# Kernel optimization log

Hardware: AMD Instinct MI355X
Metric: run time of the kernel (lower is better)

The kernel has to match this reference:

```python
import jax, jax.numpy as jnp
import numpy as np

NUM_USERS = 100000
NUM_POIS = 50000
N = NUM_USERS + NUM_POIS   # total graph nodes (users then pois)
D = 128                    # embedding_dim
POI_D = 320                # poi_embed_dim
E = 2000000                # number of edges
B = 1024                   # batch of user ids
NEG_SLOPE = 0.2


def setup_inputs() -> dict:
    key = jax.random.key(0)
    ks = jax.random.split(key, 12)
    stdv = 1.0 / np.sqrt(D)  # module resets all params to U(-stdv, stdv)
    u = lambda k, s: jax.random.uniform(k, s, jnp.float32, -stdv, stdv)
    return {
        "user_idx": jax.random.randint(ks[0], (B,), 0, NUM_USERS),
        "poi_embeddings": jax.random.normal(ks[1], (NUM_POIS, POI_D), jnp.float32),
        "edge_index": jax.random.randint(ks[2], (2, E), 0, N),
        "user_table": u(ks[3], (NUM_USERS, D)),
        "Wp": u(ks[4], (POI_D, D)), "bp": u(ks[5], (D,)),
        "W1": u(ks[6], (D, D)), "b1": u(ks[7], (D,)),
        "W2": u(ks[8], (D, D)), "b2": u(ks[9], (D,)),
        "Wf": u(ks[10], (D, D)), "bf": u(ks[11], (D,)),
    }


def _leaky(x):
    return jnp.where(x >= 0, x, NEG_SLOPE * x)


def _gcn_conv(x, W, b, src, dst, dinv):
    # PyG GCNConv: h = xW; out_i = sum_{j->i} dinv_j*dinv_i*h_j + dinv_i^2*h_i + b
    h = x @ W
    norm = dinv[src] * dinv[dst]                       # [E]
    agg = jax.ops.segment_sum(h[src] * norm[:, None], dst, num_segments=N)
    agg = agg + (dinv * dinv)[:, None] * h             # self-loop term
    return agg + b


def reference(user_idx, poi_embeddings, edge_index, user_table,
              Wp, bp, W1, b1, W2, b2, Wf, bf):
    src, dst = edge_index[0], edge_index[1]
    # degree with self-loops (edge weight 1)
    deg = 1.0 + jax.ops.segment_sum(jnp.ones((E,), jnp.float32), dst, num_segments=N)
    dinv = jax.lax.rsqrt(deg)

    poi_feats = poi_embeddings @ Wp + bp               # [NUM_POIS, D]
    x = jnp.concatenate([user_table, poi_feats], axis=0)  # [N, D]
    x = _leaky(_gcn_conv(x, W1, b1, src, dst, dinv))
    # dropout p=0.2 is identity in eval mode
    x = _leaky(_gcn_conv(x, W2, b2, src, dst, dinv))

    out = x[user_idx] + user_table[user_idx]           # [B, D]
    return out @ Wf + bf
```

## Files before the change

kernel.cpp:

```cpp
#include <hip/hip_runtime.h>

#define NUSERS 100000
#define NPOIS  50000
#define NN     150000
#define DD     128
#define EE     2000000
#define BB     1024
#define NT2M   32768

#define CH_IPT 16
#define CH_BLK 256
#define CHUNK  (CH_IPT * CH_BLK)

#define HR   3
#define HS   50000
#define HSI  12500
#define HC   85
#define HPER 23532

typedef __attribute__((ext_vector_type(8))) short short8;
typedef __attribute__((ext_vector_type(4))) float f32x4;
typedef unsigned short ushort_t;

__device__ __forceinline__ ushort_t f2bf(float x) {
    union { float f; unsigned u; } a; a.f = x;
    unsigned r = a.u + 0x7fffu + ((a.u >> 16) & 1u);
    return (ushort_t)(r >> 16);
}
__device__ __forceinline__ float bf2f(ushort_t h) {
    union { unsigned u; float f; } a; a.u = ((unsigned)h) << 16;
    return a.f;
}

__global__ void k_mark(const int* __restrict__ uidx, int* __restrict__ mask_s2,
                       int* __restrict__ mask_t2) {
    int b = blockIdx.x * blockDim.x + threadIdx.x;
    if (b < BB) { int u = uidx[b]; mask_s2[u] = 1; mask_t2[u] = 1; }
}

__global__ void k_markT2(const int* __restrict__ src, const int* __restrict__ dst,
                         const int* __restrict__ mask_s2, int* __restrict__ mask_t2) {
    const int nq = EE / 4;
    int stride = gridDim.x * blockDim.x;
    for (int q = blockIdx.x * blockDim.x + threadIdx.x; q < nq; q += stride) {
        int4 d4 = *(const int4*)&dst[q << 2];
        int m0 = mask_s2[d4.x], m1 = mask_s2[d4.y];
        int m2 = mask_s2[d4.z], m3 = mask_s2[d4.w];
        if (m0 | m1 | m2 | m3) {
            int4 s4 = *(const int4*)&src[q << 2];
            if (m0) mask_t2[s4.x] = 1;
            if (m1) mask_t2[s4.y] = 1;
            if (m2) mask_t2[s4.z] = 1;
            if (m3) mask_t2[s4.w] = 1;
        }
    }
}

__global__ __launch_bounds__(1024)
void k_hist3(const int* __restrict__ dst, int* __restrict__ slab) {
    __shared__ int h[HSI];
    const int r = blockIdx.x / HC, c = blockIdx.x % HC;
    const int lo = r * HS;
    const int tid = threadIdx.x;
    for (int i = tid; i < HSI; i += 1024) h[i] = 0;
    __syncthreads();
    const int e0 = c * HPER;
    const int e1 = min(e0 + HPER, EE);
    for (int e = e0 + tid * 4; e < e1; e += 4096) {
        int4 d4 = *(const int4*)&dst[e];
        unsigned u0 = (unsigned)(d4.x - lo), u1 = (unsigned)(d4.y - lo);
        unsigned u2 = (unsigned)(d4.z - lo), u3 = (unsigned)(d4.w - lo);
        if (u0 < (unsigned)HS) atomicAdd(&h[u0 >> 2], 1 << ((u0 & 3) << 3));
        if (u1 < (unsigned)HS) atomicAdd(&h[u1 >> 2], 1 << ((u1 & 3) << 3));
        if (u2 < (unsigned)HS) atomicAdd(&h[u2 >> 2], 1 << ((u2 & 3) << 3));
        if (u3 < (unsigned)HS) atomicAdd(&h[u3 >> 2], 1 << ((u3 & 3) << 3));
    }
    __syncthreads();
    int* out = slab + (size_t)blockIdx.x * HSI;
    for (int i = tid; i < HSI; i += 1024) out[i] = h[i];
}

__global__ void k_reduce3(const int* __restrict__ slab, int* __restrict__ cnt,
                          float* __restrict__ dinv) {
    int i = blockIdx.x * blockDim.x + threadIdx.x;
    if (i >= HR * HSI) return;
    int r = i / HSI, ii = i - r * HSI;
    const int* p = slab + (size_t)(r * HC) * HSI + ii;
    int s = 0;
    #pragma unroll
    for (int c = 0; c < HC; ++c) s += p[(size_t)c * HSI];
    int n0 = r * HS + (ii << 2);
    int4 cv;
    cv.x = s & 255; cv.y = (s >> 8) & 255; cv.z = (s >> 16) & 255; cv.w = (s >> 24) & 255;
    *(int4*)&cnt[n0] = cv;
    float4 dv;
    dv.x = rsqrtf(1.0f + (float)cv.x); dv.y = rsqrtf(1.0f + (float)cv.y);
    dv.z = rsqrtf(1.0f + (float)cv.z); dv.w = rsqrtf(1.0f + (float)cv.w);
    *(float4*)&dinv[n0] = dv;
}

__global__ __launch_bounds__(256)
void k_slots(const int* __restrict__ mask_s2, const int* __restrict__ mask_t2,
             int* __restrict__ slot_s2, int* __restrict__ slot_t2,
             int* __restrict__ rev_s2, int* __restrict__ rev_t2,
             int* __restrict__ ctr) {
    __shared__ int s_wcnt_t[4], s_wcnt_s[4];
    __shared__ int s_base_t, s_base_s;
    const int tid = threadIdx.x;
    const int lane = tid & 63;
    const int wid = tid >> 6;
    const int nch = (NN + CHUNK - 1) / CHUNK;
    for (int c = blockIdx.x; c < nch; c += gridDim.x) {
        const int n0 = c * CHUNK;
        unsigned hbits_t = 0, hbits_s = 0;
        int wt = 0, ws = 0;
        #pragma unroll
        for (int i = 0; i < CH_IPT; ++i) {
            int n = n0 + i * CH_BLK + tid;
            bool inb = (n < NN);
            bool ht = inb && (mask_t2[n] != 0);
            bool hs = inb && (mask_s2[n] != 0);
            unsigned long long mt = __ballot(ht);
            unsigned long long ms = __ballot(hs);
            if (ht) hbits_t |= (1u << i);
            if (hs) hbits_s |= (1u << i);
            wt += __popcll(mt); ws += __popcll(ms);
        }
        if (lane == 0) { s_wcnt_t[wid] = wt; s_wcnt_s[wid] = ws; }
        __syncthreads();
        if (tid == 0) s_base_t = atomicAdd(&ctr[0], s_wcnt_t[0]+s_wcnt_t[1]+s_wcnt_t[2]+s_wcnt_t[3]);
        if (tid == 1) s_base_s = atomicAdd(&ctr[1], s_wcnt_s[0]+s_wcnt_s[1]+s_wcnt_s[2]+s_wcnt_s[3]);
        __syncthreads();
        int off_t = s_base_t, off_s = s_base_s;
        for (int w = 0; w < wid; ++w) { off_t += s_wcnt_t[w]; off_s += s_wcnt_s[w]; }
        #pragma unroll
        for (int i = 0; i < CH_IPT; ++i) {
            unsigned long long mt = __ballot((hbits_t >> i) & 1);
            unsigned long long ms = __ballot((hbits_s >> i) & 1);
            int n = n0 + i * CH_BLK + tid;
            if ((hbits_t >> i) & 1) {
                int p = off_t + __popcll(mt & ((1ull << lane) - 1ull));
                slot_t2[n] = p; rev_t2[p] = n;
            }
            if ((hbits_s >> i) & 1) {
                int p = off_s + __popcll(ms & ((1ull << lane) - 1ull));
                slot_s2[n] = p; rev_s2[p] = n;
            }
            off_t += __popcll(mt); off_s += __popcll(ms);
        }
        __syncthreads();
    }
}

__global__ __launch_bounds__(1024)
void k_scan2(const int* __restrict__ ctr, const int* __restrict__ rev_t2,
             const int* __restrict__ rev_s2, const int* __restrict__ cnt,
             int* __restrict__ ptr1, int* __restrict__ cur1, int* __restrict__ cur1b,
             int* __restrict__ ptr2, int* __restrict__ cur2, int* __restrict__ cur2b) {
    __shared__ int wsum[16];
    __shared__ int s_carry;
    const int which = blockIdx.x;
    const int n = ctr[which];
    const int* rev = which ? rev_s2 : rev_t2;
    int* ptr = which ? ptr2 : ptr1;
    int* cur = which ? cur2 : cur1;
    int* curB = which ? cur2b : cur1b;
    const int tid = threadIdx.x;
    const int lane = tid & 63, wid = tid >> 6;
    if (tid == 0) s_carry = 0;
    __syncthreads();
    for (int base = 0; base < n; base += 4096) {
        int i0 = base + tid * 4;
        int v[4];
        #pragma unroll
        for (int k = 0; k < 4; ++k) {
            int i = i0 + k;
            v[k] = (i < n) ? cnt[rev[i]] : 0;
        }
        int tsum = v[0] + v[1] + v[2] + v[3];
        int x = tsum;
        #pragma unroll
        for (int s = 1; s < 64; s <<= 1) {
            int y = __shfl_up(x, s, 64);
            if (lane >= s) x += y;
        }
        if (lane == 63) wsum[wid] = x;
        __syncthreads();
        if (wid == 0) {
            int wv = (lane < 16) ? wsum[lane] : 0;
            #pragma unroll
            for (int s = 1; s < 16; s <<= 1) {
                int y = __shfl_up(wv, s, 64);
                if (lane >= s) wv += y;
            }
            if (lane < 16) wsum[lane] = wv;
        }
        __syncthreads();
        int carry = s_carry;
        int woff = (wid > 0) ? wsum[wid - 1] : 0;
        int excl = carry + woff + (x - tsum);
        #pragma unroll
        for (int k = 0; k < 4; ++k) {
            int i = i0 + k;
            if (i < n) { ptr[i] = excl; cur[i] = excl; curB[i] = excl + v[k]; }
            excl += v[k];
        }
        __syncthreads();
        if (tid == 0) s_carry = carry + wsum[15];
        __syncthreads();
    }
}

__global__ void k_scatter(const int* __restrict__ src, const int* __restrict__ dst,
                          const int* __restrict__ mask_s2, const int* __restrict__ mask_t2,
                          const int* __restrict__ slot_s2, const int* __restrict__ slot_t2,
                          int* __restrict__ cur1, int* __restrict__ cur1b,
                          int* __restrict__ cur2,
                          int* __restrict__ csr1, int* __restrict__ csr2) {
    int stride = gridDim.x * blockDim.x;
    for (int e = blockIdx.x * blockDim.x + threadIdx.x; e < EE; e += stride) {
        int d = dst[e];
        bool t = (mask_t2[d] != 0);
        bool s2 = (mask_s2[d] != 0);
        if (t | s2) {
            int s = src[e];
            if (t) {
                int sl = slot_t2[d];
                if (s < NUSERS) { int p = atomicAdd(&cur1[sl], 1);  csr1[p] = s; }
                else            { int p = atomicAdd(&cur1b[sl], -1); csr1[p - 1] = s; }
            }
            if (s2) { int p = atomicAdd(&cur2[slot_s2[d]], 1); csr2[p] = s; }
        }
    }
}

__global__ void k_wpw1(const float* __restrict__ Wp, const float* __restrict__ W1,
                       float* __restrict__ WpW1) {
    int i = blockIdx.x * blockDim.x + threadIdx.x;
    if (i >= 320 * 128) return;
    int r = i >> 7, c = i & 127;
    float s = 0.f;
    for (int k = 0; k < 128; ++k) s = fmaf(Wp[r * 128 + k], W1[k * 128 + c], s);
    WpW1[i] = s;
}

__global__ void k_bpw1(const float* __restrict__ bp, const float* __restrict__ W1,
                       float* __restrict__ bpW1) {
    int c = threadIdx.x;
    float s = 0.f;
    for (int k = 0; k < 128; ++k) s = fmaf(bp[k], W1[k * 128 + c], s);
    bpW1[c] = s;
}

__global__ void k_wprepW(const float* __restrict__ W1, const float* __restrict__ WpW1,
                         const float* __restrict__ bpW1,
                         ushort_t* __restrict__ Th, ushort_t* __restrict__ Tl) {
    int i = blockIdx.x * blockDim.x + threadIdx.x;
    if (i >= 128 * 512) return;
    int n = i >> 9, k = i & 511;
    float x = (k < 128) ? W1[k * 128 + n]
            : (k < 448) ? WpW1[(k - 128) * 128 + n]
            : (k == 448) ? bpW1[n] : 0.f;
    ushort_t h = f2bf(x);
    ushort_t l = f2bf(x - bf2f(h));
    Th[n * 512 + k] = h; Tl[n * 512 + k] = l;
}

__global__ void k_wprep2(const float* __restrict__ W2, const float* __restrict__ Wf,
                         ushort_t* __restrict__ T2h, ushort_t* __restrict__ T2l,
                         ushort_t* __restrict__ Tfh, ushort_t* __restrict__ Tfl) {
    int i = blockIdx.x * blockDim.x + threadIdx.x;
    if (i >= 2 * 128 * 128) return;
    int wsel = i >> 14, j = i & 16383;
    const float* W = wsel ? Wf : W2;
    ushort_t* Th = wsel ? Tfh : T2h;
    ushort_t* Tl = wsel ? Tfl : T2l;
    int k = j >> 7, n = j & 127;
    float x = W[j];
    ushort_t h = f2bf(x);
    ushort_t l = f2bf(x - bf2f(h));
    Th[n * 128 + k] = h; Tl[n * 128 + k] = l;
}

__global__ __launch_bounds__(256)
void k_agg1(const int* __restrict__ ctr, const int* __restrict__ rev_t2,
            const int* __restrict__ ptr1, const int* __restrict__ cur1,
            const int* __restrict__ cnt, const int* __restrict__ csr1,
            const float* __restrict__ dinv,
            const float* __restrict__ ut, const float* __restrict__ poi,
            ushort_t* __restrict__ Ah, ushort_t* __restrict__ Al) {
    const int nt2 = min(ctr[0], NT2M);
    const int lane = threadIdx.x & 63;
    const int w0 = (blockIdx.x * blockDim.x + threadIdx.x) >> 6;
    const int nw = (gridDim.x * blockDim.x) >> 6;
    for (int slot = w0; slot < nt2; slot += nw) {
        int node = rev_t2[slot];
        float dn = dinv[node], dd = dn * dn;
        float u0 = 0.f, u1 = 0.f, p0 = 0.f, p1 = 0.f, p2 = 0.f, p3 = 0.f, p4 = 0.f, sP = 0.f;
        if (node < NUSERS) {
            const float2 v = *(const float2*)&ut[((size_t)node << 7) + (lane << 1)];
            u0 = dd * v.x; u1 = dd * v.y;
        } else {
            const float* pr = poi + (size_t)(node - NUSERS) * 320;
            p0 = dd * pr[lane]; p1 = dd * pr[lane + 64]; p2 = dd * pr[lane + 128];
            p3 = dd * pr[lane + 192]; p4 = dd * pr[lane + 256];
            sP = dd;
        }
        const int j0 = ptr1[slot];
        const int sp = cur1[slot];
        const int jend = j0 + cnt[node];
        int j = j0;
        for (; j + 4 <= sp; j += 4) {
            int s0 = csr1[j], s1 = csr1[j + 1], s2 = csr1[j + 2], s3 = csr1[j + 3];
            float w0 = dinv[s0] * dn, w1 = dinv[s1] * dn;
            float w2 = dinv[s2] * dn, w3 = dinv[s3] * dn;
            const float2 v0 = *(const float2*)&ut[((size_t)s0 << 7) + (lane << 1)];
            const float2 v1 = *(const float2*)&ut[((size_t)s1 << 7) + (lane << 1)];
            const float2 v2 = *(const float2*)&ut[((size_t)s2 << 7) + (lane << 1)];
            const float2 v3 = *(const float2*)&ut[((size_t)s3 << 7) + (lane << 1)];
            u0 = fmaf(w0, v0.x, u0); u1 = fmaf(w0, v0.y, u1);
            u0 = fmaf(w1, v1.x, u0); u1 = fmaf(w1, v1.y, u1);
            u0 = fmaf(w2, v2.x, u0); u1 = fmaf(w2, v2.y, u1);
            u0 = fmaf(w3, v3.x, u0); u1 = fmaf(w3, v3.y, u1);
        }
        for (; j < sp; ++j) {
            int s = csr1[j];
            float w = dinv[s] * dn;
            const float2 v = *(const float2*)&ut[((size_t)s << 7) + (lane << 1)];
            u0 = fmaf(w, v.x, u0); u1 = fmaf(w, v.y, u1);
        }
        for (j = sp; j + 2 <= jend; j += 2) {
            int s0 = csr1[j], s1 = csr1[j + 1];
            float w0 = dinv[s0] * dn, w1 = dinv[s1] * dn;
            const float* pa = poi + (size_t)(s0 - NUSERS) * 320;
            const float* pb = poi + (size_t)(s1 - NUSERS) * 320;
            p0 = fmaf(w0, pa[lane], p0);       p1 = fmaf(w0, pa[lane + 64], p1);
            p2 = fmaf(w0, pa[lane + 128], p2); p3 = fmaf(w0, pa[lane + 192], p3);
            p4 = fmaf(w0, pa[lane + 256], p4);
            p0 = fmaf(w1, pb[lane], p0);       p1 = fmaf(w1, pb[lane + 64], p1);
            p2 = fmaf(w1, pb[lane + 128], p2); p3 = fmaf(w1, pb[lane + 192], p3);
            p4 = fmaf(w1, pb[lane + 256], p4);
            sP += w0 + w1;
        }
        for (; j < jend; ++j) {
            int s = csr1[j];
            float w = dinv[s] * dn;
            const float* pr = poi + (size_t)(s - NUSERS) * 320;
            p0 = fmaf(w, pr[lane], p0);       p1 = fmaf(w, pr[lane + 64], p1);
            p2 = fmaf(w, pr[lane + 128], p2); p3 = fmaf(w, pr[lane + 192], p3);
            p4 = fmaf(w, pr[lane + 256], p4);
            sP += w;
        }
        size_t base = (size_t)slot << 9;
        ushort_t h, l;
        h = f2bf(u0); l = f2bf(u0 - bf2f(h));
        Ah[base + (lane << 1)] = h; Al[base + (lane << 1)] = l;
        h = f2bf(u1); l = f2bf(u1 - bf2f(h));
        Ah[base + (lane << 1) + 1] = h; Al[base + (lane << 1) + 1] = l;
        float pv[5] = {p0, p1, p2, p3, p4};
        #pragma unroll
        for (int q = 0; q < 5; ++q) {
            h = f2bf(pv[q]); l = f2bf(pv[q] - bf2f(h));
            Ah[base + 128 + lane + (q << 6)] = h; Al[base + 128 + lane + (q << 6)] = l;
        }
        float t = (lane == 0) ? sP : 0.f;
        h = f2bf(t); l = f2bf(t - bf2f(h));
        Ah[base + 448 + lane] = h; Al[base + 448 + lane] = l;
    }
}

template<int KSTEPS, bool LEAKY>
__global__ __launch_bounds__(256)
void gemm_bf(const ushort_t* __restrict__ Ah_g, const ushort_t* __restrict__ Al_g,
             const ushort_t* __restrict__ BTh, const ushort_t* __restrict__ BTl,
             const float* __restrict__ bias, float* __restrict__ C,
             int M, const int* __restrict__ Mdyn)
{
    constexpr int K = KSTEPS * 64;
    __shared__ ushort_t Bh[128 * 64], Bl[128 * 64];
    __shared__ ushort_t Ahs[64 * 64], Als[64 * 64];
    const int tid = threadIdx.x;
    const int wave = tid >> 6, lane = tid & 63;
    const int wr = wave >> 1, wc = wave & 1;
    const int lr = lane & 15, g = lane >> 4;
    if (Mdyn) M = min(*Mdyn, NT2M);
    const int ntiles = (M + 63) >> 6;
    for (int tile = blockIdx.x; tile < ntiles; tile += gridDim.x) {
        const int row0 = tile << 6;
        f32x4 acc[2][4];
        #pragma unroll
        for (int a = 0; a < 2; ++a)
            #pragma unroll
            for (int b = 0; b < 4; ++b) acc[a][b] = (f32x4){0.f, 0.f, 0.f, 0.f};
        for (int kc = 0; kc < K; kc += 64) {
            __syncthreads();
            #pragma unroll
            for (int i = 0; i < 4; ++i) {
                int c = tid + i * 256;
                int n = c >> 3, kq = c & 7;
                size_t go = (size_t)n * K + kc + kq * 8;
                int boff = n * 128 + ((kq * 16) ^ ((n & 7) << 4));
                *(int4*)((char*)Bh + boff) = *(const int4*)&BTh[go];
                *(int4*)((char*)Bl + boff) = *(const int4*)&BTl[go];
            }
            #pragma unroll
            for (int i = 0; i < 2; ++i) {
                int c = tid + i * 256;
                int r = c >> 3, kq = c & 7;
                int row = row0 + r;
                int4 va = {0, 0, 0, 0}, vb = {0, 0, 0, 0};
                if (row < M) {
                    size_t go = (size_t)row * K + kc + kq * 8;
                    va = *(const int4*)&Ah_g[go];
                    vb = *(const int4*)&Al_g[go];
                }
                int aoff = r * 128 + ((kq * 16) ^ ((r & 7) << 4));
                *(int4*)((char*)Ahs + aoff) = va;
                *(int4*)((char*)Als + aoff) = vb;
            }
            __syncthreads();
            #pragma unroll
            for (int kk2 = 0; kk2 < 2; ++kk2) {
                short8 afh[2], afl[2];
                #pragma unroll
                for (int rt = 0; rt < 2; ++rt) {
                    int ar = wr * 32 + rt * 16 + lr;
                    int off = ar * 128 + ((kk2 * 64 + g * 16) ^ ((ar & 7) << 4));
                    afh[rt] = *(short8*)((char*)Ahs + off);
                    afl[rt] = *(short8*)((char*)Als + off);
                }
                #pragma unroll
                for (int ct = 0; ct < 4; ++ct) {
                    int bn = wc * 64 + ct * 16 + lr;
                    int off = bn * 128 + ((kk2 * 64 + g * 16) ^ ((bn & 7) << 4));
                    short8 bfh = *(short8*)((char*)Bh + off);
                    short8 bfl = *(short8*)((char*)Bl + off);
                    #pragma unroll
                    for (int rt = 0; rt < 2; ++rt) {
                        acc[rt][ct] = __builtin_amdgcn_mfma_f32_16x16x32_bf16(afh[rt], bfh, acc[rt][ct], 0, 0, 0);
                        acc[rt][ct] = __builtin_amdgcn_mfma_f32_16x16x32_bf16(afh[rt], bfl, acc[rt][ct], 0, 0, 0);
                        acc[rt][ct] = __builtin_amdgcn_mfma_f32_16x16x32_bf16(afl[rt], bfh, acc[rt][ct], 0, 0, 0);
                    }
                }
            }
        }
        #pragma unroll
        for (int ct = 0; ct < 4; ++ct) {
            int col = wc * 64 + ct * 16 + lr;
            float bv = bias[col];
            #pragma unroll
            for (int rt = 0; rt < 2; ++rt) {
                #pragma unroll
                for (int v = 0; v < 4; ++v) {
                    int row = row0 + wr * 32 + rt * 16 + g * 4 + v;
                    if (row < M) {
                        float o = acc[rt][ct][v] + bv;
                        if (LEAKY) o = o >= 0.f ? o : 0.2f * o;
                        C[(size_t)row * 128 + col] = o;
                    }
                }
            }
        }
    }
}

__global__ __launch_bounds__(256)
void k_agg2(const int* __restrict__ ctr, const int* __restrict__ rev_s2,
            const int* __restrict__ ptr2, const int* __restrict__ cnt,
            const int* __restrict__ csr2, const int* __restrict__ slot_t2,
            const float* __restrict__ dinv, const float* __restrict__ x1c,
            ushort_t* __restrict__ X2h, ushort_t* __restrict__ X2l) {
    const int ns2 = ctr[1];
    const int lane = threadIdx.x & 63;
    const int col = lane << 1;
    const int w0 = (blockIdx.x * blockDim.x + threadIdx.x) >> 6;
    const int nw = (gridDim.x * blockDim.x) >> 6;
    for (int slot = w0; slot < ns2; slot += nw) {
        int node = rev_s2[slot];
        float dn = dinv[node], dd = dn * dn;
        float2 acc = *(const float2*)&x1c[((size_t)slot_t2[node] << 7) + col];
        acc.x *= dd; acc.y *= dd;
        const int j0 = ptr2[slot];
        const int jend = j0 + cnt[node];
        int j = j0;
        for (; j + 4 <= jend; j += 4) {
            int s0 = csr2[j], s1 = csr2[j + 1], s2 = csr2[j + 2], s3 = csr2[j + 3];
            float w0 = dinv[s0] * dn, w1 = dinv[s1] * dn;
            float w2 = dinv[s2] * dn, w3 = dinv[s3] * dn;
            const float2 h0 = *(const float2*)&x1c[((size_t)slot_t2[s0] << 7) + col];
            const float2 h1 = *(const float2*)&x1c[((size_t)slot_t2[s1] << 7) + col];
            const float2 h2 = *(const float2*)&x1c[((size_t)slot_t2[s2] << 7) + col];
            const float2 h3 = *(const float2*)&x1c[((size_t)slot_t2[s3] << 7) + col];
            acc.x = fmaf(w0, h0.x, acc.x); acc.y = fmaf(w0, h0.y, acc.y);
            acc.x = fmaf(w1, h1.x, acc.x); acc.y = fmaf(w1, h1.y, acc.y);
            acc.x = fmaf(w2, h2.x, acc.x); acc.y = fmaf(w2, h2.y, acc.y);
            acc.x = fmaf(w3, h3.x, acc.x); acc.y = fmaf(w3, h3.y, acc.y);
        }
        for (; j < jend; ++j) {
            int s = csr2[j];
            float w = dinv[s] * dn;
            const float2 h = *(const float2*)&x1c[((size_t)slot_t2[s] << 7) + col];
            acc.x = fmaf(w, h.x, acc.x);
            acc.y = fmaf(w, h.y, acc.y);
        }
        size_t base = ((size_t)slot << 7) + col;
        ushort_t h0 = f2bf(acc.x), l0 = f2bf(acc.x - bf2f(h0));
        ushort_t h1 = f2bf(acc.y), l1 = f2bf(acc.y - bf2f(h1));
        X2h[base] = h0; X2h[base + 1] = h1;
        X2l[base] = l0; X2l[base + 1] = l1;
    }
}

__global__ void k_finalA(const int* __restrict__ uidx, const int* __restrict__ slot_s2,
                         const float* __restrict__ x2c, const float* __restrict__ ut,
                         ushort_t* __restrict__ Fh, ushort_t* __restrict__ Fl) {
    int i = blockIdx.x * blockDim.x + threadIdx.x;
    if (i >= BB * 64) return;
    int b = i >> 6, l = i & 63;
    int u = uidx[b];
    const float2 xv = *(const float2*)&x2c[((size_t)slot_s2[u] << 7) + (l << 1)];
    const float2 uv = *(const float2*)&ut[((size_t)u << 7) + (l << 1)];
    float a0 = xv.x + uv.x, a1 = xv.y + uv.y;
    size_t base = ((size_t)b << 7) + (l << 1);
    ushort_t h0 = f2bf(a0), l0 = f2bf(a0 - bf2f(h0));
    ushort_t h1 = f2bf(a1), l1 = f2bf(a1 - bf2f(h1));
    Fh[base] = h0; Fh[base + 1] = h1;
    Fl[base] = l0; Fl[base + 1] = l1;
}

extern "C" void kernel_launch(void* const* d_in, const int* in_sizes, int n_in,
                              void* d_out, int out_size, void* d_ws, size_t ws_size,
                              hipStream_t stream) {
    const int*   uidx    = (const int*)d_in[0];
    const float* poi     = (const float*)d_in[1];
    const int*   src     = (const int*)d_in[2];
    const int*   dst     = ((const int*)d_in[2]) + EE;
    const float* usert   = (const float*)d_in[3];
    const float* Wp      = (const float*)d_in[4];
    const float* bp      = (const float*)d_in[5];
    const float* W1      = (const float*)d_in[6];
    const float* b1      = (const float*)d_in[7];
    const float* W2      = (const float*)d_in[8];
    const float* b2      = (const float*)d_in[9];
    const float* Wf      = (const float*)d_in[10];
    const float* bf      = (const float*)d_in[11];
    float* out = (float*)d_out;

    char* w = (char*)d_ws;
    size_t off = 0;
    auto alloc = [&](size_t bytes) -> void* {
        void* p = w + off;
        off = (off + bytes + 255) & ~(size_t)255;
        return p;
    };
    float* dinv    = (float*)alloc((size_t)NN * 4);
    int*   cnt     = (int*)  alloc((size_t)NN * 4);
    int*   mask_s2 = (int*)  alloc((size_t)NN * 4);
    int*   mask_t2 = (int*)  alloc((size_t)NN * 4);
    int*   slot_s2 = (int*)  alloc((size_t)NN * 4);
    int*   slot_t2 = (int*)  alloc((size_t)NN * 4);
    int*   rev_t2  = (int*)  alloc((size_t)NN * 4);
    int*   rev_s2  = (int*)  alloc((size_t)BB * 4);
    int*   ptr1    = (int*)  alloc((size_t)(NN + 1) * 4);
    int*   cur1    = (int*)  alloc((size_t)(NN + 1) * 4);
    int*   cur1b   = (int*)  alloc((size_t)(NN + 1) * 4);
    int*   ptr2    = (int*)  alloc((size_t)(BB + 2) * 4);
    int*   cur2    = (int*)  alloc((size_t)(BB + 2) * 4);
    int*   cur2b   = (int*)  alloc((size_t)(BB + 2) * 4);
    int*   ctr     = (int*)  alloc(256);
    int*   csr1    = (int*)  alloc((size_t)EE * 4);
    int*   csr2    = (int*)  alloc((size_t)EE * 4);
    int*   slab    = (int*)  alloc((size_t)HR * HC * HSI * 4);
    float* WpW1    = (float*)alloc((size_t)320 * 128 * 4);
    float* bpW1    = (float*)alloc((size_t)128 * 4);
    ushort_t* WTh  = (ushort_t*)alloc((size_t)128 * 512 * 2);
    ushort_t* WTl  = (ushort_t*)alloc((size_t)128 * 512 * 2);
    ushort_t* W2Th = (ushort_t*)alloc((size_t)128 * 128 * 2);
    ushort_t* W2Tl = (ushort_t*)alloc((size_t)128 * 128 * 2);
    ushort_t* WfTh = (ushort_t*)alloc((size_t)128 * 128 * 2);
    ushort_t* WfTl = (ushort_t*)alloc((size_t)128 * 128 * 2);
    ushort_t* Ah   = (ushort_t*)alloc((size_t)NT2M * 512 * 2);
    ushort_t* Al   = (ushort_t*)alloc((size_t)NT2M * 512 * 2);
    float* x1c     = (float*)alloc((size_t)NT2M * 128 * 4);
    ushort_t* X2h  = (ushort_t*)alloc((size_t)2048 * 128 * 2);
    ushort_t* X2l  = (ushort_t*)alloc((size_t)2048 * 128 * 2);
    float* x2c     = (float*)alloc((size_t)2048 * 128 * 4);
    ushort_t* Fh   = (ushort_t*)alloc((size_t)BB * 128 * 2);
    ushort_t* Fl   = (ushort_t*)alloc((size_t)BB * 128 * 2);
    if (off > ws_size) return;

    hipMemsetAsync(mask_s2, 0, (size_t)NN * 4, stream);
    hipMemsetAsync(mask_t2, 0, (size_t)NN * 4, stream);
    hipMemsetAsync(ctr, 0, 256, stream);

    k_wpw1  <<<160, 256, 0, stream>>>(Wp, W1, WpW1);
    k_bpw1  <<<1, 128, 0, stream>>>(bp, W1, bpW1);
    k_wprepW<<<256, 256, 0, stream>>>(W1, WpW1, bpW1, WTh, WTl);
    k_wprep2<<<128, 256, 0, stream>>>(W2, Wf, W2Th, W2Tl, WfTh, WfTl);

    k_mark   <<<(BB + 255) / 256, 256, 0, stream>>>(uidx, mask_s2, mask_t2);
    k_markT2 <<<2048, 256, 0, stream>>>(src, dst, mask_s2, mask_t2);
    k_hist3  <<<HR * HC, 1024, 0, stream>>>(dst, slab);
    k_reduce3<<<(HR * HSI + 255) / 256, 256, 0, stream>>>(slab, cnt, dinv);

    k_slots<<<(NN + CHUNK - 1) / CHUNK, 256, 0, stream>>>(mask_s2, mask_t2, slot_s2, slot_t2,
                                                          rev_s2, rev_t2, ctr);
    k_scan2<<<2, 1024, 0, stream>>>(ctr, rev_t2, rev_s2, cnt,
                                    ptr1, cur1, cur1b, ptr2, cur2, cur2b);
    k_scatter<<<2048, 256, 0, stream>>>(src, dst, mask_s2, mask_t2, slot_s2, slot_t2,
                                        cur1, cur1b, cur2, csr1, csr2);

    k_agg1<<<2048, 256, 0, stream>>>(ctr, rev_t2, ptr1, cur1, cnt, csr1, dinv,
                                     usert, poi, Ah, Al);
    gemm_bf<8, true><<<240, 256, 0, stream>>>(Ah, Al, WTh, WTl, b1, x1c, 0, ctr + 0);

    k_agg2<<<256, 256, 0, stream>>>(ctr, rev_s2, ptr2, cnt, csr2, slot_t2, dinv, x1c, X2h, X2l);
    gemm_bf<2, true><<<16, 256, 0, stream>>>(X2h, X2l, W2Th, W2Tl, b2, x2c, 0, ctr + 1);

    k_finalA<<<(BB * 64 + 255) / 256, 256, 0, stream>>>(uidx, slot_s2, x2c, usert, Fh, Fl);
    gemm_bf<2, false><<<16, 256, 0, stream>>>(Fh, Fl, WfTh, WfTl, bf, out, BB, nullptr);
}
```

Measured before the change: 195.7 us.

## Fuse T2 marking into histogram kernel and use slot sentinels in scatter

Removes the standalone k_markT2 pass and folds the mask_s2->mask_t2 propagation into k_hist3. Each of its three row-blocks handles a third of its edge chunk, which saves one launch and reuses the dst stream the kernel already reads. k_scatter now reads slot_t2/slot_s2 directly, with slots memset to -1 beforehand, so the mask lookups go away. This relies on k_slots writing slots only for marked nodes. The aggregation loops drop their scalar tail loops in favour of clamped, predicated 4-wide (or 3-wide for POIs) bodies. Risks include two extra 600KB memsets and some wasted loads on padded lanes.

```diff
diff --git a/kernel.cpp b/kernel.cpp
--- a/kernel.cpp
+++ b/kernel.cpp
@@ -38,26 +38,10 @@
     if (b < BB) { int u = uidx[b]; mask_s2[u] = 1; mask_t2[u] = 1; }
 }
 
-__global__ void k_markT2(const int* __restrict__ src, const int* __restrict__ dst,
-                         const int* __restrict__ mask_s2, int* __restrict__ mask_t2) {
-    const int nq = EE / 4;
-    int stride = gridDim.x * blockDim.x;
-    for (int q = blockIdx.x * blockDim.x + threadIdx.x; q < nq; q += stride) {
-        int4 d4 = *(const int4*)&dst[q << 2];
-        int m0 = mask_s2[d4.x], m1 = mask_s2[d4.y];
-        int m2 = mask_s2[d4.z], m3 = mask_s2[d4.w];
-        if (m0 | m1 | m2 | m3) {
-            int4 s4 = *(const int4*)&src[q << 2];
-            if (m0) mask_t2[s4.x] = 1;
-            if (m1) mask_t2[s4.y] = 1;
-            if (m2) mask_t2[s4.z] = 1;
-            if (m3) mask_t2[s4.w] = 1;
-        }
-    }
-}
-
 __global__ __launch_bounds__(1024)
-void k_hist3(const int* __restrict__ dst, int* __restrict__ slab) {
+void k_hist3(const int* __restrict__ src, const int* __restrict__ dst,
+             const int* __restrict__ mask_s2, int* __restrict__ mask_t2,
+             int* __restrict__ slab) {
     __shared__ int h[HSI];
     const int r = blockIdx.x / HC, c = blockIdx.x % HC;
     const int lo = r * HS;
@@ -74,6 +58,20 @@
         if (u1 < (unsigned)HS) atomicAdd(&h[u1 >> 2], 1 << ((u1 & 3) << 3));
         if (u2 < (unsigned)HS) atomicAdd(&h[u2 >> 2], 1 << ((u2 & 3) << 3));
         if (u3 < (unsigned)HS) atomicAdd(&h[u3 >> 2], 1 << ((u3 & 3) << 3));
+    }
+    const int m0 = e0 + r * (HPER / 3);
+    const int m1 = min(e0 + (r + 1) * (HPER / 3), EE);
+    for (int e = m0 + tid * 4; e < m1; e += 4096) {
+        int4 d4 = *(const int4*)&dst[e];
+        int q0 = mask_s2[d4.x], q1 = mask_s2[d4.y];
+        int q2 = mask_s2[d4.z], q3 = mask_s2[d4.w];
+        if (q0 | q1 | q2 | q3) {
+            int4 s4 = *(const int4*)&src[e];
+            if (q0) mask_t2[s4.x] = 1;
+            if (q1) mask_t2[s4.y] = 1;
+            if (q2) mask_t2[s4.z] = 1;
+            if (q3) mask_t2[s4.w] = 1;
+        }
     }
     __syncthreads();
     int* out = slab + (size_t)blockIdx.x * HSI;
@@ -212,7 +210,6 @@
 }
 
 __global__ void k_scatter(const int* __restrict__ src, const int* __restrict__ dst,
-                          const int* __restrict__ mask_s2, const int* __restrict__ mask_t2,
                           const int* __restrict__ slot_s2, const int* __restrict__ slot_t2,
                           int* __restrict__ cur1, int* __restrict__ cur1b,
                           int* __restrict__ cur2,
@@ -220,16 +217,17 @@
     int stride = gridDim.x * blockDim.x;
     for (int e = blockIdx.x * blockDim.x + threadIdx.x; e < EE; e += stride) {
         int d = dst[e];
-        bool t = (mask_t2[d] != 0);
-        bool s2 = (mask_s2[d] != 0);
-        if (t | s2) {
-            int s = src[e];
-            if (t) {
-                int sl = slot_t2[d];
-                if (s < NUSERS) { int p = atomicAdd(&cur1[sl], 1);  csr1[p] = s; }
-                else            { int p = atomicAdd(&cur1b[sl], -1); csr1[p - 1] = s; }
-            }
-            if (s2) { int p = atomicAdd(&cur2[slot_s2[d]], 1); csr2[p] = s; }
+        int sl1 = slot_t2[d];
+        int sl2 = slot_s2[d];
+        if ((sl1 | sl2) != -1 || sl1 >= 0 || sl2 >= 0) {
+            if (sl1 >= 0 || sl2 >= 0) {
+                int s = src[e];
+                if (sl1 >= 0) {
+                    if (s < NUSERS) { int p = atomicAdd(&cur1[sl1], 1);   csr1[p] = s; }
+                    else            { int p = atomicAdd(&cur1b[sl1], -1); csr1[p - 1] = s; }
+                }
+                if (sl2 >= 0) { int p = atomicAdd(&cur2[sl2], 1); csr2[p] = s; }
+            }
         }
     }
 }
@@ -291,9 +289,9 @@
             ushort_t* __restrict__ Ah, ushort_t* __restrict__ Al) {
     const int nt2 = min(ctr[0], NT2M);
     const int lane = threadIdx.x & 63;
-    const int w0 = (blockIdx.x * blockDim.x + threadIdx.x) >> 6;
+    const int w0id = (blockIdx.x * blockDim.x + threadIdx.x) >> 6;
     const int nw = (gridDim.x * blockDim.x) >> 6;
-    for (int slot = w0; slot < nt2; slot += nw) {
+    for (int slot = w0id; slot < nt2; slot += nw) {
         int node = rev_t2[slot];
         float dn = dinv[node], dd = dn * dn;
         float u0 = 0.f, u1 = 0.f, p0 = 0.f, p1 = 0.f, p2 = 0.f, p3 = 0.f, p4 = 0.f, sP = 0.f;
@@ -309,11 +307,13 @@
         const int j0 = ptr1[slot];
         const int sp = cur1[slot];
         const int jend = j0 + cnt[node];
-        int j = j0;
-        for (; j + 4 <= sp; j += 4) {
-            int s0 = csr1[j], s1 = csr1[j + 1], s2 = csr1[j + 2], s3 = csr1[j + 3];
-            float w0 = dinv[s0] * dn, w1 = dinv[s1] * dn;
-            float w2 = dinv[s2] * dn, w3 = dinv[s3] * dn;
+        for (int j = j0; j < sp; j += 4) {
+            int i1 = min(j + 1, sp - 1), i2 = min(j + 2, sp - 1), i3 = min(j + 3, sp - 1);
+            int s0 = csr1[j], s1 = csr1[i1], s2 = csr1[i2], s3 = csr1[i3];
+            float w0 = dn * dinv[s0];
+            float w1 = (j + 1 < sp) ? dn * dinv[s1] : 0.f;
+            float w2 = (j + 2 < sp) ? dn * dinv[s2] : 0.f;
+            float w3 = (j + 3 < sp) ? dn * dinv[s3] : 0.f;
             const float2 v0 = *(const float2*)&ut[((size_t)s0 << 7) + (lane << 1)];
             const float2 v1 = *(const float2*)&ut[((size_t)s1 << 7) + (lane << 1)];
             const float2 v2 = *(const float2*)&ut[((size_t)s2 << 7) + (lane << 1)];
@@ -323,33 +323,25 @@
             u0 = fmaf(w2, v2.x, u0); u1 = fmaf(w2, v2.y, u1);
             u0 = fmaf(w3, v3.x, u0); u1 = fmaf(w3, v3.y, u1);
         }
-        for (; j < sp; ++j) {
-            int s = csr1[j];
-            float w = dinv[s] * dn;
-            const float2 v = *(const float2*)&ut[((size_t)s << 7) + (lane << 1)];
-            u0 = fmaf(w, v.x, u0); u1 = fmaf(w, v.y, u1);
-        }
-        for (j = sp; j + 2 <= jend; j += 2) {
-            int s0 = csr1[j], s1 = csr1[j + 1];
-            float w0 = dinv[s0] * dn, w1 = dinv[s1] * dn;
+        for (int j = sp; j < jend; j += 3) {
+            int i1 = min(j + 1, jend - 1), i2 = min(j + 2, jend - 1);
+            int s0 = csr1[j], s1 = csr1[i1], s2 = csr1[i2];
+            float w0 = dn * dinv[s0];
+            float w1 = (j + 1 < jend) ? dn * dinv[s1] : 0.f;
+            float w2 = (j + 2 < jend) ? dn * dinv[s2] : 0.f;
             const float* pa = poi + (size_t)(s0 - NUSERS) * 320;
             const float* pb = poi + (size_t)(s1 - NUSERS) * 320;
+            const float* pc = poi + (size_t)(s2 - NUSERS) * 320;
             p0 = fmaf(w0, pa[lane], p0);       p1 = fmaf(w0, pa[lane + 64], p1);
             p2 = fmaf(w0, pa[lane + 128], p2); p3 = fmaf(w0, pa[lane + 192], p3);
             p4 = fmaf(w0, pa[lane + 256], p4);
             p0 = fmaf(w1, pb[lane], p0);       p1 = fmaf(w1, pb[lane + 64], p1);
             p2 = fmaf(w1, pb[lane + 128], p2); p3 = fmaf(w1, pb[lane + 192], p3);
             p4 = fmaf(w1, pb[lane + 256], p4);
-            sP += w0 + w1;
-        }
-        for (; j < jend; ++j) {
-            int s = csr1[j];
-            float w = dinv[s] * dn;
-            const float* pr = poi + (size_t)(s - NUSERS) * 320;
-            p0 = fmaf(w, pr[lane], p0);       p1 = fmaf(w, pr[lane + 64], p1);
-            p2 = fmaf(w, pr[lane + 128], p2); p3 = fmaf(w, pr[lane + 192], p3);
-            p4 = fmaf(w, pr[lane + 256], p4);
-            sP += w;
+            p0 = fmaf(w2, pc[lane], p0);       p1 = fmaf(w2, pc[lane + 64], p1);
+            p2 = fmaf(w2, pc[lane + 128], p2); p3 = fmaf(w2, pc[lane + 192], p3);
+            p4 = fmaf(w2, pc[lane + 256], p4);
+            sP += w0 + w1 + w2;
         }
         size_t base = (size_t)slot << 9;
         ushort_t h, l;
@@ -473,20 +465,22 @@
     const int ns2 = ctr[1];
     const int lane = threadIdx.x & 63;
     const int col = lane << 1;
-    const int w0 = (blockIdx.x * blockDim.x + threadIdx.x) >> 6;
+    const int w0id = (blockIdx.x * blockDim.x + threadIdx.x) >> 6;
     const int nw = (gridDim.x * blockDim.x) >> 6;
-    for (int slot = w0; slot < ns2; slot += nw) {
+    for (int slot = w0id; slot < ns2; slot += nw) {
         int node = rev_s2[slot];
         float dn = dinv[node], dd = dn * dn;
         float2 acc = *(const float2*)&x1c[((size_t)slot_t2[node] << 7) + col];
         acc.x *= dd; acc.y *= dd;
         const int j0 = ptr2[slot];
         const int jend = j0 + cnt[node];
-        int j = j0;
-        for (; j + 4 <= jend; j += 4) {
-            int s0 = csr2[j], s1 = csr2[j + 1], s2 = csr2[j + 2], s3 = csr2[j + 3];
-            float w0 = dinv[s0] * dn, w1 = dinv[s1] * dn;
-            float w2 = dinv[s2] * dn, w3 = dinv[s3] * dn;
+        for (int j = j0; j < jend; j += 4) {
+            int i1 = min(j + 1, jend - 1), i2 = min(j + 2, jend - 1), i3 = min(j + 3, jend - 1);
+            int s0 = csr2[j], s1 = csr2[i1], s2 = csr2[i2], s3 = csr2[i3];
+            float w0 = dn * dinv[s0];
+            float w1 = (j + 1 < jend) ? dn * dinv[s1] : 0.f;
+            float w2 = (j + 2 < jend) ? dn * dinv[s2] : 0.f;
+            float w3 = (j + 3 < jend) ? dn * dinv[s3] : 0.f;
             const float2 h0 = *(const float2*)&x1c[((size_t)slot_t2[s0] << 7) + col];
             const float2 h1 = *(const float2*)&x1c[((size_t)slot_t2[s1] << 7) + col];
             const float2 h2 = *(const float2*)&x1c[((size_t)slot_t2[s2] << 7) + col];
@@ -495,13 +489,6 @@
             acc.x = fmaf(w1, h1.x, acc.x); acc.y = fmaf(w1, h1.y, acc.y);
             acc.x = fmaf(w2, h2.x, acc.x); acc.y = fmaf(w2, h2.y, acc.y);
             acc.x = fmaf(w3, h3.x, acc.x); acc.y = fmaf(w3, h3.y, acc.y);
-        }
-        for (; j < jend; ++j) {
-            int s = csr2[j];
-            float w = dinv[s] * dn;
-            const float2 h = *(const float2*)&x1c[((size_t)slot_t2[s] << 7) + col];
-            acc.x = fmaf(w, h.x, acc.x);
-            acc.y = fmaf(w, h.y, acc.y);
         }
         size_t base = ((size_t)slot << 7) + col;
         ushort_t h0 = f2bf(acc.x), l0 = f2bf(acc.x - bf2f(h0));
@@ -591,6 +578,8 @@
 
     hipMemsetAsync(mask_s2, 0, (size_t)NN * 4, stream);
     hipMemsetAsync(mask_t2, 0, (size_t)NN * 4, stream);
+    hipMemsetAsync(slot_s2, 0xFF, (size_t)NN * 4, stream);
+    hipMemsetAsync(slot_t2, 0xFF, (size_t)NN * 4, stream);
     hipMemsetAsync(ctr, 0, 256, stream);
 
     k_wpw1  <<<160, 256, 0, stream>>>(Wp, W1, WpW1);
@@ -599,15 +588,14 @@
     k_wprep2<<<128, 256, 0, stream>>>(W2, Wf, W2Th, W2Tl, WfTh, WfTl);
 
     k_mark   <<<(BB + 255) / 256, 256, 0, stream>>>(uidx, mask_s2, mask_t2);
-    k_markT2 <<<2048, 256, 0, stream>>>(src, dst, mask_s2, mask_t2);
-    k_hist3  <<<HR * HC, 1024, 0, stream>>>(dst, slab);
+    k_hist3  <<<HR * HC, 1024, 0, stream>>>(src, dst, mask_s2, mask_t2, slab);
     k_reduce3<<<(HR * HSI + 255) / 256, 256, 0, stream>>>(slab, cnt, dinv);
 
     k_slots<<<(NN + CHUNK - 1) / CHUNK, 256, 0, stream>>>(mask_s2, mask_t2, slot_s2, slot_t2,
                                                           rev_s2, rev_t2, ctr);
     k_scan2<<<2, 1024, 0, stream>>>(ctr, rev_t2, rev_s2, cnt,
                                     ptr1, cur1, cur1b, ptr2, cur2, cur2b);
-    k_scatter<<<2048, 256, 0, stream>>>(src, dst, mask_s2, mask_t2, slot_s2, slot_t2,
+    k_scatter<<<2048, 256, 0, stream>>>(src, dst, slot_s2, slot_t2,
                                         cur1, cur1b, cur2, csr1, csr2);
 
     k_agg1<<<2048, 256, 0, stream>>>(ctr, rev_t2, ptr1, cur1, cnt, csr1, dinv,
```

After: 201.7 us. 1.03x slower.
